# Performance work log

Measured on AMD Instinct MI355X. Metric: run time of the kernel, lower is better.

Reference implementation:

```python
import jax, jax.numpy as jnp
import numpy as np

SCALING = 128.0 / 256.0  # lora_alpha / r
EPS = 1e-8


def setup_inputs() -> dict:
    key = jax.random.key(0)
    ks = jax.random.split(key, 7)
    B, S, D = 4, 2048, 4096
    R = 256
    return {
        "x": jax.random.normal(ks[0], (B, S, D), dtype=jnp.float32),
        "base_weight": jax.random.normal(ks[1], (D, D), dtype=jnp.float32) * 0.02,
        "bias": jax.random.normal(ks[2], (D,), dtype=jnp.float32) * 0.02,
        "lora_A": jax.random.normal(ks[3], (R, D), dtype=jnp.float32) * 0.02,
        "lora_B": jax.random.normal(ks[4], (D, R), dtype=jnp.float32) * 0.02,
        "magnitude": jax.random.uniform(ks[5], (D, 1), dtype=jnp.float32) + 0.5,
        "turkish_weights": jax.random.normal(ks[6], (D, 1), dtype=jnp.float32),
    }


def reference(x, base_weight, bias, lora_A, lora_B, magnitude, turkish_weights):
    # DoRA weight: W = m * (W0 + scaling * B @ A) / ||.||_row * turkish
    combined = base_weight + SCALING * (lora_B @ lora_A)          # [out, in]
    row_norm = jnp.linalg.norm(combined, axis=1, keepdims=True)   # [out, 1]
    dora_w = magnitude * (combined / (row_norm + EPS))
    dora_w = dora_w * turkish_weights
    # dropout is identity in eval mode
    out = jnp.einsum("bsd,od->bso", x, dora_w) + bias
    return out
```

## Files before the change

### kernel.cpp

```cpp
#include <hip/hip_runtime.h>

typedef _Float16 f16;
typedef _Float16 f16x8 __attribute__((ext_vector_type(8)));
typedef float f32x4 __attribute__((ext_vector_type(4)));

__device__ __forceinline__ void gload_lds16(const void* g, void* l) {
  __builtin_amdgcn_global_load_lds((const __attribute__((address_space(1))) void*)g,
                                   (__attribute__((address_space(3))) void*)l, 16, 0, 0);
}

__device__ __forceinline__ f32x4 mfma16(f16x8 a, f16x8 b, f32x4 c) {
  return __builtin_amdgcn_mfma_f32_16x16x32_f16(a, b, c, 0, 0, 0);
}


__global__ void k_cvt(const float* __restrict__ src, f16* __restrict__ dst, int n8) {
  int i = blockIdx.x * 256 + threadIdx.x;
  if (i >= n8) return;
  const float4* s4 = reinterpret_cast<const float4*>(src) + (size_t)i * 2;
  float4 a = s4[0], b = s4[1];
  f16x8 v;
  v[0] = (f16)a.x; v[1] = (f16)a.y; v[2] = (f16)a.z; v[3] = (f16)a.w;
  v[4] = (f16)b.x; v[5] = (f16)b.y; v[6] = (f16)b.z; v[7] = (f16)b.w;
  *reinterpret_cast<f16x8*>(dst + (size_t)i * 8) = v;
}

__global__ void k_cvt_at(const float* __restrict__ A, f16* __restrict__ at) {
  __shared__ float t[64][65];
  int bi = blockIdx.x, br = blockIdx.y;
  int tx = threadIdx.x & 63, ty = threadIdx.x >> 6;
#pragma unroll
  for (int p = 0; p < 16; ++p) {
    int r = p * 4 + ty;
    t[r][tx] = A[(size_t)(br * 64 + r) * 4096 + bi * 64 + tx];
  }
  __syncthreads();
#pragma unroll
  for (int p = 0; p < 16; ++p) {
    int i = p * 4 + ty;
    at[(size_t)(bi * 64 + i) * 256 + br * 64 + tx] = (f16)t[tx][i];
  }
}

__device__ __forceinline__ void stage_tile_lin(const f16* __restrict__ g, size_t row0, int k0,
                                               int ldg, f16* s, int wid, int lane) {
#pragma unroll
  for (int t = 0; t < 4; ++t) {
    int c = (wid * 4 + t) * 64 + lane;
    const f16* gp = g + (row0 + (size_t)(c >> 3)) * (size_t)ldg + k0 + (c & 7) * 8;
    gload_lds16(gp, s + (wid * 4 + t) * 512);
  }
}

__global__ __launch_bounds__(256) void k_lora(const f16* __restrict__ bh,
                                              const f16* __restrict__ at,
                                              const float* __restrict__ base,
                                              f16* __restrict__ ch,
                                              float* __restrict__ partial) {
  __shared__ f16 sA[128 * 64];
  __shared__ f16 sB[128 * 64];
  __shared__ float ssum[2][128];
  int tid = threadIdx.x;
  int wid = tid >> 6, lane = tid & 63;
  int wm = wid >> 1, wn = wid & 1;
  int ln = lane & 15, q = lane >> 4;
  int bm = blockIdx.x >> 5, bn = blockIdx.x & 31;
  int brow = bm * 128, bcol = bn * 128;
  f32x4 acc[4][4] = {};
  for (int kt = 0; kt < 256; kt += 64) {
    __syncthreads();
    stage_tile_lin(bh, brow, kt, 256, sA, wid, lane);
    stage_tile_lin(at, bcol, kt, 256, sB, wid, lane);
    __syncthreads();
#pragma unroll
    for (int ks = 0; ks < 2; ++ks) {
      f16x8 af[4], bf[4];
#pragma unroll
      for (int mi = 0; mi < 4; ++mi)
        af[mi] = *reinterpret_cast<const f16x8*>(&sA[(wm * 64 + mi * 16 + ln) * 64 + ks * 32 + q * 8]);
#pragma unroll
      for (int ni = 0; ni < 4; ++ni)
        bf[ni] = *reinterpret_cast<const f16x8*>(&sB[(wn * 64 + ni * 16 + ln) * 64 + ks * 32 + q * 8]);
#pragma unroll
      for (int mi = 0; mi < 4; ++mi)
#pragma unroll
        for (int ni = 0; ni < 4; ++ni)
          acc[mi][ni] = mfma16(af[mi], bf[ni], acc[mi][ni]);
    }
  }
#pragma unroll
  for (int mi = 0; mi < 4; ++mi) {
#pragma unroll
    for (int j = 0; j < 4; ++j) {
      int row = brow + wm * 64 + mi * 16 + q * 4 + j;
      float s = 0.f;
#pragma unroll
      for (int ni = 0; ni < 4; ++ni) {
        int col = bcol + wn * 64 + ni * 16 + ln;
        float v = base[(size_t)row * 4096 + col] + 0.5f * acc[mi][ni][j];
        ch[(size_t)row * 4096 + col] = (f16)v;
        s += v * v;
      }
#pragma unroll
      for (int m = 1; m < 16; m <<= 1) s += __shfl_xor(s, m, 64);
      if (ln == 0) ssum[wn][wm * 64 + mi * 16 + q * 4 + j] = s;
    }
  }
  __syncthreads();
  if (tid < 128) {
    float p = ssum[0][tid] + ssum[1][tid];
    partial[(size_t)(brow + tid) * 32 + bn] = p;
  }
}

__global__ void k_scale(const float* __restrict__ partial, const float* __restrict__ mag,
                        const float* __restrict__ turk, float* __restrict__ scale) {
  int o = blockIdx.x * 256 + threadIdx.x;
  float s = 0.f;
#pragma unroll
  for (int c = 0; c < 32; ++c) s += partial[(size_t)o * 32 + c];
  scale[o] = mag[o] * turk[o] / (sqrtf(s) + 1e-8f);
}


__device__ __forceinline__ void stage2(const f16* p, f16* d) {
  gload_lds16(p, d);
  gload_lds16(p + 32768, d + 512);
}

__device__ __forceinline__ void lda4(const f16* base, int g, int ln, int sw, f16x8 (&af)[4]) {
#pragma unroll
  for (int f = 0; f < 4; ++f)
    af[f] = *reinterpret_cast<const f16x8*>(base + (g * 64 + f * 16 + ln) * 64 + sw);
}

__device__ __forceinline__ void ldb4(const f16* base, int ln, int sw, f16x8 (&bf)[4]) {
#pragma unroll
  for (int n = 0; n < 4; ++n)
    bf[n] = *reinterpret_cast<const f16x8*>(base + (n * 16 + ln) * 64 + sw);
}

template <int G>
__device__ __forceinline__ void mfma16x(f16x8 (&af)[4], f16x8 (&bf)[4], f32x4 (&acc)[8][4]) {
#pragma unroll
  for (int f = 0; f < 4; ++f)
#pragma unroll
    for (int n = 0; n < 4; ++n)
      acc[G * 4 + f][n] = mfma16(af[f], bf[n], acc[G * 4 + f][n]);
}

__global__ __launch_bounds__(512, 2) void k_main(const f16* __restrict__ xh,
                                                 const f16* __restrict__ ch,
                                                 const float* __restrict__ scale,
                                                 const float* __restrict__ bias,
                                                 float* __restrict__ out) {
  __shared__ __align__(16) f16 sA[32768];
  __shared__ __align__(16) f16 sB[32768];
  int tid = threadIdx.x;
  int wid = tid >> 6, lane = tid & 63;
  int wm = wid >> 2, wn = wid & 3;
  int ln = lane & 15, q8 = lane >> 4;
  int sw0 = (q8 ^ (ln & 7)) * 8;
  int sw1 = ((4 + q8) ^ (ln & 7)) * 8;

  int bid = blockIdx.x;
  int swz = (bid & 7) * 64 + (bid >> 3);
  int bm = swz >> 4, bn = swz & 15;
  size_t brow = (size_t)bm * 256;
  int bcol = bn * 256;

  f32x4 acc[8][4] = {};
  f16x8 af0[4], af1[4], af2[4], af3[4], bf0[4], bf1[4];

  const int aOff = wm * 8192;
  const int bOff = (wn >> 1) * 8192 + (wn & 1) * 4096;

  int rloc = wid * 16 + (lane >> 3);
  int swcol = ((lane & 7) ^ ((lane >> 3) & 7)) * 8;
  const f16* pa0 = xh + (brow + rloc) * 4096 + swcol;
  const f16* pa1 = pa0 + 128 * 4096;
  const f16* pb0 = ch + ((size_t)bcol + rloc) * 4096 + swcol;
  const f16* pb1 = pb0 + 128 * 4096;
  f16* myA = sA + wid * 1024;
  f16* myB = sB + wid * 1024;

  stage2(pa0, myA);
  stage2(pa1, myA + 8192);
  stage2(pb0, myB);
  stage2(pb1, myB + 8192);
  stage2(pa1 + 64, myA + 16384 + 8192);
  stage2(pa0 + 64, myA + 16384);
  pa0 += 128; pa1 += 128; pb0 += 64; pb1 += 64;
  asm volatile("s_waitcnt vmcnt(4)");
  __builtin_amdgcn_s_barrier();

#define KTILE(CUR, SB, SA, WVM)                                                              \
  {                                                                                          \
    const int NC = (CUR) ^ 1;                                                                \
    const f16* cA = sA + (CUR) * 16384 + aOff;                                               \
    const f16* cB = sB + (CUR) * 16384 + bOff;                                               \
                                      \
    lda4(cA, 0, ln, sw0, af0); ldb4(cB, ln, sw0, bf0);                                       \
    if (SB) { stage2(pb0, myB + NC * 16384); pb0 += 64; }                                    \
    __builtin_amdgcn_s_barrier();                                                            \
    asm volatile("s_waitcnt lgkmcnt(0)");                                                    \
    __builtin_amdgcn_s_setprio(1); mfma16x<0>(af0, bf0, acc); __builtin_amdgcn_s_setprio(0); \
    __builtin_amdgcn_s_barrier();                                                            \
                                      \
    lda4(cA, 0, ln, sw1, af1); ldb4(cB, ln, sw1, bf1);                                       \
    if (SB) { stage2(pb1, myB + NC * 16384 + 8192); pb1 += 64; }                             \
    __builtin_amdgcn_s_barrier();                                                            \
    asm volatile("s_waitcnt lgkmcnt(0)");                                                    \
    __builtin_amdgcn_s_setprio(1); mfma16x<0>(af1, bf1, acc); __builtin_amdgcn_s_setprio(0); \
    __builtin_amdgcn_s_barrier();                                                            \
                                                                     \
    lda4(cA, 1, ln, sw0, af2);                                                               \
    __builtin_amdgcn_s_barrier();                                                            \
    asm volatile("s_waitcnt lgkmcnt(0)");                                                    \
    __builtin_amdgcn_s_setprio(1); mfma16x<1>(af2, bf0, acc); __builtin_amdgcn_s_setprio(0); \
    __builtin_amdgcn_s_barrier();                                                            \
                \
    lda4(cA, 1, ln, sw1, af3);                                                               \
    if (SA) { stage2(pa1, myA + (CUR) * 16384 + 8192); pa1 += 64;                            \
              stage2(pa0, myA + (CUR) * 16384);        pa0 += 64; }                          \
    __builtin_amdgcn_s_barrier();                                                            \
    asm volatile("s_waitcnt lgkmcnt(0)");                                                    \
    __builtin_amdgcn_s_setprio(1); mfma16x<1>(af3, bf1, acc); __builtin_amdgcn_s_setprio(0); \
    asm volatile(WVM);                                                                       \
    __builtin_amdgcn_s_barrier();                                                            \
  }

  for (int t = 0; t < 62; t += 2) {
    KTILE(0, 1, 1, "s_waitcnt vmcnt(4)")
    KTILE(1, 1, 1, "s_waitcnt vmcnt(4)")
  }
  KTILE(0, 1, 0, "s_waitcnt vmcnt(0)")
  KTILE(1, 0, 0, "")
#undef KTILE

#pragma unroll
  for (int n = 0; n < 4; ++n) {
    int col = bcol + wn * 64 + n * 16 + ln;
    float sc = scale[col], bs = bias[col];
#pragma unroll
    for (int mf = 0; mf < 8; ++mf)
#pragma unroll
      for (int j = 0; j < 4; ++j) {
        size_t row = brow + wm * 128 + mf * 16 + q8 * 4 + j;
        out[row * 4096 + col] = sc * acc[mf][n][j] + bs;
      }
  }
}

extern "C" void kernel_launch(void* const* d_in, const int* in_sizes, int n_in,
                              void* d_out, int out_size, void* d_ws, size_t ws_size,
                              hipStream_t stream) {
  const float* x    = (const float*)d_in[0];
  const float* base = (const float*)d_in[1];
  const float* bias = (const float*)d_in[2];
  const float* lA   = (const float*)d_in[3];
  const float* lB   = (const float*)d_in[4];
  const float* mag  = (const float*)d_in[5];
  const float* turk = (const float*)d_in[6];
  float* out = (float*)d_out;
  char* ws = (char*)d_ws;

  f16*   xh      = (f16*)(ws);
  f16*   ch      = (f16*)(ws + 67108864);
  f16*   at      = (f16*)(ws + 100663296);
  f16*   bh      = (f16*)(ws + 102760448);
  float* partial = (float*)(ws + 104857600);
  float* scale   = (float*)(ws + 105381888);

  k_cvt<<<16384, 256, 0, stream>>>(x, xh, 4194304);
  k_cvt<<<512, 256, 0, stream>>>(lB, bh, 131072);
  k_cvt_at<<<dim3(64, 4), 256, 0, stream>>>(lA, at);
  k_lora<<<1024, 256, 0, stream>>>(bh, at, base, ch, partial);
  k_scale<<<16, 256, 0, stream>>>(partial, mag, turk, scale);
  k_main<<<512, 512, 0, stream>>>(xh, ch, scale, bias, out);
}
```

Before: 368.9 us.

## Software-pipeline LDS fragment loads with MFMA using ping-pong register buffers

Restructures the K-tile loop so each LDS fragment load for the next sub-step is issued before the MFMA block of the current sub-step, using two alternating register fragment sets instead of four. The next tile's first fragments are prefetched at the end of each tile. It also drops several barriers. This aims to hide LDS read latency behind matrix math and cut synchronisation stalls, at the cost of tighter ordering constraints and possible register pressure or hazards on the reused LDS buffers.

```diff
diff --git a/kernel.cpp b/kernel.cpp
--- a/kernel.cpp
+++ b/kernel.cpp
@@ -170,7 +170,7 @@
   int bcol = bn * 256;
 
   f32x4 acc[8][4] = {};
-  f16x8 af0[4], af1[4], af2[4], af3[4], bf0[4], bf1[4];
+  f16x8 afA[4], afB[4], bfA[4], bfB[4];
 
   const int aOff = wm * 8192;
   const int bOff = (wn >> 1) * 8192 + (wn & 1) * 4096;
@@ -193,40 +193,46 @@
   pa0 += 128; pa1 += 128; pb0 += 64; pb1 += 64;
   asm volatile("s_waitcnt vmcnt(4)");
   __builtin_amdgcn_s_barrier();
+  __builtin_amdgcn_sched_barrier(0);
+  lda4(sA + aOff, 0, ln, sw0, afA);
+  ldb4(sB + bOff, ln, sw0, bfA);
 
 #define KTILE(CUR, SB, SA, WVM)                                                              \
   {                                                                                          \
     const int NC = (CUR) ^ 1;                                                                \
     const f16* cA = sA + (CUR) * 16384 + aOff;                                               \
     const f16* cB = sB + (CUR) * 16384 + bOff;                                               \
-                                      \
-    lda4(cA, 0, ln, sw0, af0); ldb4(cB, ln, sw0, bf0);                                       \
+    const f16* nA = sA + NC * 16384 + aOff;                                                  \
+    const f16* nB = sB + NC * 16384 + bOff;                                                  \
+                             \
+    asm volatile("s_waitcnt lgkmcnt(0)");                                                    \
+    __builtin_amdgcn_sched_barrier(0);                                                       \
+    lda4(cA, 0, ln, sw1, afB); ldb4(cB, ln, sw1, bfB);                                       \
     if (SB) { stage2(pb0, myB + NC * 16384); pb0 += 64; }                                    \
-    __builtin_amdgcn_s_barrier();                                                            \
-    asm volatile("s_waitcnt lgkmcnt(0)");                                                    \
-    __builtin_amdgcn_s_setprio(1); mfma16x<0>(af0, bf0, acc); __builtin_amdgcn_s_setprio(0); \
-    __builtin_amdgcn_s_barrier();                                                            \
-                                      \
-    lda4(cA, 0, ln, sw1, af1); ldb4(cB, ln, sw1, bf1);                                       \
+    __builtin_amdgcn_s_setprio(1); mfma16x<0>(afA, bfA, acc); __builtin_amdgcn_s_setprio(0); \
+    __builtin_amdgcn_s_barrier();                                                            \
+                            \
+    asm volatile("s_waitcnt lgkmcnt(0)");                                                    \
+    __builtin_amdgcn_sched_barrier(0);                                                       \
+    lda4(cA, 1, ln, sw0, afA);                                                               \
     if (SB) { stage2(pb1, myB + NC * 16384 + 8192); pb1 += 64; }                             \
-    __builtin_amdgcn_s_barrier();                                                            \
-    asm volatile("s_waitcnt lgkmcnt(0)");                                                    \
-    __builtin_amdgcn_s_setprio(1); mfma16x<0>(af1, bf1, acc); __builtin_amdgcn_s_setprio(0); \
-    __builtin_amdgcn_s_barrier();                                                            \
-                                                                     \
-    lda4(cA, 1, ln, sw0, af2);                                                               \
-    __builtin_amdgcn_s_barrier();                                                            \
-    asm volatile("s_waitcnt lgkmcnt(0)");                                                    \
-    __builtin_amdgcn_s_setprio(1); mfma16x<1>(af2, bf0, acc); __builtin_amdgcn_s_setprio(0); \
-    __builtin_amdgcn_s_barrier();                                                            \
-                \
-    lda4(cA, 1, ln, sw1, af3);                                                               \
+    __builtin_amdgcn_s_setprio(1); mfma16x<0>(afB, bfB, acc); __builtin_amdgcn_s_setprio(0); \
+    __builtin_amdgcn_s_barrier();                                                            \
+                    \
+    asm volatile("s_waitcnt lgkmcnt(0)");                                                    \
+    __builtin_amdgcn_sched_barrier(0);                                                       \
+    lda4(cA, 1, ln, sw1, afB);                                                               \
+    __builtin_amdgcn_s_setprio(1); mfma16x<1>(afA, bfA, acc); __builtin_amdgcn_s_setprio(0); \
+    asm volatile("s_waitcnt lgkmcnt(0)");                                                    \
+    __builtin_amdgcn_s_barrier();                                                            \
+               \
     if (SA) { stage2(pa1, myA + (CUR) * 16384 + 8192); pa1 += 64;                            \
               stage2(pa0, myA + (CUR) * 16384);        pa0 += 64; }                          \
-    __builtin_amdgcn_s_barrier();                                                            \
-    asm volatile("s_waitcnt lgkmcnt(0)");                                                    \
-    __builtin_amdgcn_s_setprio(1); mfma16x<1>(af3, bf1, acc); __builtin_amdgcn_s_setprio(0); \
     asm volatile(WVM);                                                                       \
+    __builtin_amdgcn_s_barrier();                                                            \
+    __builtin_amdgcn_sched_barrier(0);                                                       \
+    lda4(nA, 0, ln, sw0, afA); ldb4(nB, ln, sw0, bfA);                                       \
+    __builtin_amdgcn_s_setprio(1); mfma16x<1>(afB, bfB, acc); __builtin_amdgcn_s_setprio(0); \
     __builtin_amdgcn_s_barrier();                                                            \
   }
 
```

After: 390.2 us. 1.06x slower.
